# Optimization experiments

Measured on AMD Instinct MI355X. Metric: run time of the kernel, lower is better.

Reference implementation:

```python
import jax, jax.numpy as jnp
import numpy as np

B, S, D = 4, 128, 4096
H, KV, HD = 32, 8, 128
REP = H // KV  # GQA repeat factor = 4


def setup_inputs() -> dict:
    key = jax.random.key(0)
    ks = jax.random.split(key, 10)
    scale = 0.02
    x = jax.random.normal(ks[0], (B, S, D), dtype=jnp.float32)
    # projection weights stored as (in, out) so y = x @ W + b (== torch Linear)
    wq = jax.random.normal(ks[1], (D, H * HD), dtype=jnp.float32) * scale
    bq = jax.random.normal(ks[2], (H * HD,), dtype=jnp.float32) * scale
    wk = jax.random.normal(ks[3], (D, KV * HD), dtype=jnp.float32) * scale
    bk = jax.random.normal(ks[4], (KV * HD,), dtype=jnp.float32) * scale
    wv = jax.random.normal(ks[5], (D, KV * HD), dtype=jnp.float32) * scale
    bv = jax.random.normal(ks[6], (KV * HD,), dtype=jnp.float32) * scale
    wo = jax.random.normal(ks[7], (H * HD, D), dtype=jnp.float32) * scale
    bo = jax.random.normal(ks[8], (D,), dtype=jnp.float32) * scale
    # rotary frequencies: theta=10000, half-dim = HD//2 = 64
    inv_freq = 1.0 / (10000.0 ** (jnp.arange(0, HD, 2, dtype=jnp.float32) / HD))
    t = jnp.arange(S, dtype=jnp.float32)
    angles = jnp.outer(t, inv_freq)  # (S, 64)
    freqs_cos = jnp.cos(angles)
    freqs_sin = jnp.sin(angles)
    # additive causal mask (S, S): 0 on/below diagonal, -inf above
    mask = jnp.where(jnp.tril(jnp.ones((S, S), dtype=bool)), 0.0, -jnp.inf).astype(jnp.float32)
    cache_k = jnp.zeros((B, S, KV, HD), dtype=jnp.float32)
    cache_v = jnp.zeros((B, S, KV, HD), dtype=jnp.float32)
    return {
        "x": x, "start_pos": 0, "freqs_cos": freqs_cos, "freqs_sin": freqs_sin,
        "mask": mask, "cache_k": cache_k, "cache_v": cache_v,
        "wq": wq, "bq": bq, "wk": wk, "bk": bk, "wv": wv, "bv": bv,
        "wo": wo, "bo": bo,
    }


def _rope(t, cos, sin):
    # t: (B, S, h, HD); treat last dim as HD//2 complex pairs (real, imag)
    tr = t.reshape(*t.shape[:-1], HD // 2, 2)
    tre, tim = tr[..., 0], tr[..., 1]
    c = cos[None, :, None, :]  # (1, S, 1, HD//2)
    s = sin[None, :, None, :]
    out_re = tre * c - tim * s
    out_im = tre * s + tim * c
    return jnp.stack([out_re, out_im], axis=-1).reshape(t.shape)


def reference(x, start_pos, freqs_cos, freqs_sin, mask, cache_k, cache_v,
              wq, bq, wk, bk, wv, bv, wo, bo):
    bsz, seq_len, _ = x.shape
    q = (x @ wq + bq).reshape(bsz, seq_len, H, HD)
    k = (x @ wk + bk).reshape(bsz, seq_len, KV, HD)
    v = (x @ wv + bv).reshape(bsz, seq_len, KV, HD)
    q = _rope(q, freqs_cos, freqs_sin)
    k = _rope(k, freqs_cos, freqs_sin)
    # KV-cache append (functional)
    cache_k = cache_k.at[:bsz, start_pos:start_pos + seq_len].set(k)
    cache_v = cache_v.at[:bsz, start_pos:start_pos + seq_len].set(v)
    keys = cache_k[:bsz, :start_pos + seq_len]    # (B, T, KV, HD)
    vals = cache_v[:bsz, :start_pos + seq_len]
    # GQA head expansion (repeat_interleave on head dim)
    keys = jnp.repeat(keys, REP, axis=2)          # (B, T, H, HD)
    vals = jnp.repeat(vals, REP, axis=2)
    scale = 1.0 / jnp.sqrt(jnp.float32(HD))
    scores = jnp.einsum('bqhd,bkhd->bhqk', q, keys) * scale + mask
    attn = jax.nn.softmax(scores, axis=-1)
    out = jnp.einsum('bhqk,bkhd->bqhd', attn, vals).reshape(bsz, seq_len, H * HD)
    return out @ wo + bo
```

## Files before the change

kernel.cpp:

```cpp
#include <hip/hip_runtime.h>
#include <math.h>


#define B_   4
#define S_   128
#define D_   4096
#define H_   32
#define KV_  8
#define HD_  128
#define M_   (B_ * S_)
#define NQKV 6144
#define SCALE_ 0.088388347648318447f

typedef _Float16 half_t;
typedef half_t f16x8 __attribute__((ext_vector_type(8)));
typedef float  f32x4 __attribute__((ext_vector_type(4)));

__device__ inline void load_lds16(const void* g, void* l) {
    __builtin_amdgcn_global_load_lds((const __attribute__((address_space(1))) void*)g,
                                     (__attribute__((address_space(3))) void*)l,
                                     16, 0, 0);
}

__global__ void convert_f16(const float* __restrict__ in, half_t* __restrict__ out,
                            int total4) {
    int i = blockIdx.x * 256 + threadIdx.x;
    if (i >= total4) return;
    float4 f = ((const float4*)in)[i];
    __align__(8) half_t h4[4] = {(half_t)f.x, (half_t)f.y, (half_t)f.z, (half_t)f.w};
    ((uint2*)out)[i] = *(uint2*)h4;
}

__global__ __launch_bounds__(256)
void transpose_wf16(const float* __restrict__ wq, const float* __restrict__ wk,
                    const float* __restrict__ wv, half_t* __restrict__ Wt) {
    __shared__ __align__(16) float tile[64][132];
    const int t = threadIdx.x;
    const int nt = blockIdx.x, k0 = blockIdx.y * 64;
    const float* src; int Nsrc, nsrc0, ndst0;
    if (nt < 32)      { src = wq; Nsrc = 4096; nsrc0 = nt * 128;        ndst0 = nt * 128; }
    else if (nt < 40) { src = wk; Nsrc = 1024; nsrc0 = (nt - 32) * 128; ndst0 = 4096 + (nt - 32) * 128; }
    else              { src = wv; Nsrc = 1024; nsrc0 = (nt - 40) * 128; ndst0 = 5120 + (nt - 40) * 128; }
#pragma unroll
    for (int p = 0; p < 8; ++p) {
        int idx = t + p * 256;
        int r = idx >> 5, c4 = idx & 31;
        *(float4*)&tile[r][c4 * 4] =
            *(const float4*)&src[(size_t)(k0 + r) * Nsrc + nsrc0 + c4 * 4];
    }
    __syncthreads();
    const int n = t >> 1, kh = t & 1;
    __align__(16) half_t hs[32];
#pragma unroll
    for (int i = 0; i < 32; ++i)
        hs[i] = (half_t)tile[kh * 32 + i][n];
    size_t ob = (size_t)(ndst0 + n) * 4096 + k0 + kh * 32;
#pragma unroll
    for (int u = 0; u < 4; ++u)
        *(uint4*)&Wt[ob + u * 8] = *(uint4*)&hs[u * 8];
}

__global__ __launch_bounds__(256, 3)
void gemm_f16(const half_t* __restrict__ A16, const half_t* __restrict__ Bt,
              float* __restrict__ Part, int N, int K, int kslice) {
    __shared__ __align__(16) half_t As[128][64];
    __shared__ __align__(16) half_t Bs[128][64];
    const int tid = threadIdx.x;
    const int m0 = blockIdx.y * 128, n0 = blockIdx.x * 128;
    const int kbase = blockIdx.z * kslice;
    const int lane = tid & 63;
    const int quad = lane >> 4, l16 = lane & 15;
    const int w = tid >> 6;
    const int wm = (w & 1) * 64, wn = (w >> 1) * 64;
    const int tB = tid & 192;

    f32x4 acc[4][4] = {};

    for (int kc = kbase; kc < kbase + kslice; kc += 64) {
#pragma unroll
        for (int p = 0; p < 4; ++p) {
            int tb = p * 256 + tB;
            int task = tb + lane;
            int r = task >> 3;
            int os = (task ^ r) & 7;
            load_lds16(&A16[(size_t)(m0 + r) * K + kc + os * 8], (half_t*)As + tb * 8);
            load_lds16(&Bt [(size_t)(n0 + r) * K + kc + os * 8], (half_t*)Bs + tb * 8);
        }
        __syncthreads();
#pragma unroll
        for (int kk = 0; kk < 2; ++kk) {
            f16x8 af[4], bf[4];
#pragma unroll
            for (int i = 0; i < 4; ++i) {
                int ra = wm + i * 16 + l16;
                int rb = wn + i * 16 + l16;
                int L = kk * 4 + quad;
                af[i] = *(const f16x8*)&As[ra][(L ^ (ra & 7)) * 8];
                bf[i] = *(const f16x8*)&Bs[rb][(L ^ (rb & 7)) * 8];
            }
#pragma unroll
            for (int i = 0; i < 4; ++i)
#pragma unroll
                for (int j = 0; j < 4; ++j)
                    acc[i][j] = __builtin_amdgcn_mfma_f32_16x16x32_f16(af[i], bf[j], acc[i][j], 0, 0, 0);
        }
        __syncthreads();
    }
    float* Cp = Part + (size_t)blockIdx.z * ((size_t)M_ * N);
#pragma unroll
    for (int i = 0; i < 4; ++i)
#pragma unroll
        for (int j = 0; j < 4; ++j) {
            int col = n0 + wn + j * 16 + l16;
            int rowb = m0 + wm + i * 16 + quad * 4;
#pragma unroll
            for (int rg = 0; rg < 4; ++rg)
                Cp[(size_t)(rowb + rg) * N + col] = acc[i][j][rg];
        }
}

__global__ void qkv_reduce_rope(const float* __restrict__ Part, int nz,
                                const float* __restrict__ bq, const float* __restrict__ bk,
                                const float* __restrict__ bv,
                                const float* __restrict__ fc, const float* __restrict__ fs,
                                half_t* __restrict__ q16, half_t* __restrict__ k16,
                                half_t* __restrict__ vt16) {
    const int row = blockIdx.y;
    const int col = (blockIdx.x * 256 + threadIdx.x) * 2;
    const size_t off = (size_t)row * NQKV + col;
    float2 s = *(const float2*)&Part[off];
    for (int z = 1; z < nz; ++z) {
        float2 p = *(const float2*)&Part[(size_t)z * (M_ * NQKV) + off];
        s.x += p.x; s.y += p.y;
    }
    float2 bi;
    if (col < 4096)      bi = *(const float2*)&bq[col];
    else if (col < 5120) bi = *(const float2*)&bk[col - 4096];
    else                 bi = *(const float2*)&bv[col - 5120];
    s.x += bi.x; s.y += bi.y;
    if (col < 5120) {
        int d2 = (col >> 1) & 63;
        int i = row & 127;
        float c = fc[i * 64 + d2], sn = fs[i * 64 + d2];
        float re = s.x, im = s.y;
        s.x = re * c - im * sn;
        s.y = re * sn + im * c;
    }
    __align__(4) half_t hh[2] = {(half_t)s.x, (half_t)s.y};
    if (col < 4096) {
        *(unsigned int*)&q16[(size_t)row * 4096 + col] = *(unsigned int*)hh;
    } else if (col < 5120) {
        *(unsigned int*)&k16[(size_t)row * 1024 + (col - 4096)] = *(unsigned int*)hh;
    } else {
        int c = col - 5120;
        int kv = c >> 7, d = c & 127;
        int b = row >> 7, i = row & 127;
        size_t base = ((size_t)(b * 8 + kv) * 128 + d) * 128 + i;
        vt16[base]       = hh[0];
        vt16[base + 128] = hh[1];
    }
}

__global__ __launch_bounds__(256, 2)
void fused_attn(const half_t* __restrict__ q16, const half_t* __restrict__ k16,
                const half_t* __restrict__ vt16, half_t* __restrict__ a16) {
    __shared__ __align__(16) half_t Qs[32][136];
    __shared__ __align__(16) half_t Ks[128][136];
    __shared__ float Ps[32][132];
    __shared__ float red[32][16];

    const int tid = threadIdx.x;
    const int qi = blockIdx.x & 3, h = (blockIdx.x >> 2) & 31, b = blockIdx.x >> 7;
    const int kv = h >> 2;
    const int qbase = qi * 32;
    const int lane = tid & 63, w = tid >> 6;
    const int quad = lane >> 4, l16 = lane & 15;
    const int m0 = (w & 1) * 16, half64 = (w >> 1) * 64;

#pragma unroll
    for (int p = 0; p < 2; ++p) {
        int task = tid + p * 256;
        int r = task >> 4, c = task & 15;
        *(uint4*)&Qs[r][c * 8] =
            *(const uint4*)&q16[((size_t)(b * 128 + qbase + r) * 32 + h) * 128 + c * 8];
    }
#pragma unroll
    for (int p = 0; p < 8; ++p) {
        int task = tid + p * 256;
        int r = task >> 4, c = task & 15;
        *(uint4*)&Ks[r][c * 8] =
            *(const uint4*)&k16[((size_t)(b * 128 + r) * 8 + kv) * 128 + c * 8];
    }
    __syncthreads();

    f32x4 s[4] = {};
#pragma unroll
    for (int kc = 0; kc < 4; ++kc) {
        f16x8 af = *(const f16x8*)&Qs[m0 + l16][kc * 32 + quad * 8];
#pragma unroll
        for (int jb = 0; jb < 4; ++jb) {
            f16x8 bf = *(const f16x8*)&Ks[half64 + jb * 16 + l16][kc * 32 + quad * 8];
            s[jb] = __builtin_amdgcn_mfma_f32_16x16x32_f16(af, bf, s[jb], 0, 0, 0);
        }
    }
#pragma unroll
    for (int jb = 0; jb < 4; ++jb) {
        int j = half64 + jb * 16 + l16;
#pragma unroll
        for (int rg = 0; rg < 4; ++rg) {
            int row = m0 + quad * 4 + rg;
            Ps[row][j] = (j <= qbase + row) ? s[jb][rg] * SCALE_ : -1e30f;
        }
    }
    __syncthreads();

    const int r = tid >> 3, seg = tid & 7;
    float mx = -1e30f;
#pragma unroll
    for (int i = 0; i < 16; ++i) mx = fmaxf(mx, Ps[r][seg * 16 + i]);
    red[r][seg] = mx;
    __syncthreads();

    uint4 vstage[8];
#pragma unroll
    for (int p = 0; p < 8; ++p) {
        int task = tid + p * 256;
        int rr = task >> 4, c = task & 15;
        vstage[p] = *(const uint4*)&vt16[((size_t)(b * 8 + kv) * 128 + rr) * 128 + c * 8];
    }
    float m = red[r][0];
#pragma unroll
    for (int i = 1; i < 8; ++i) m = fmaxf(m, red[r][i]);
    float sum = 0.f;
#pragma unroll
    for (int i = 0; i < 16; ++i) {
        float e = __expf(Ps[r][seg * 16 + i] - m);
        Ps[r][seg * 16 + i] = e;
        sum += e;
    }
    red[r][8 + seg] = sum;
#pragma unroll
    for (int p = 0; p < 8; ++p) {
        int task = tid + p * 256;
        int rr = task >> 4, c = task & 15;
        *(uint4*)&Ks[rr][c * 8] = vstage[p];
    }
    __syncthreads();

    float tot = 0.f;
#pragma unroll
    for (int i = 0; i < 8; ++i) tot += red[r][8 + i];
    float inv = 1.0f / tot;
#pragma unroll
    for (int i = 0; i < 16; ++i)
        Qs[r][seg * 16 + i] = (half_t)(Ps[r][seg * 16 + i] * inv);
    __syncthreads();

    f32x4 o[4] = {};
#pragma unroll
    for (int jc = 0; jc < 4; ++jc) {
        f16x8 af = *(const f16x8*)&Qs[m0 + l16][jc * 32 + quad * 8];
#pragma unroll
        for (int db = 0; db < 4; ++db) {
            f16x8 bf = *(const f16x8*)&Ks[half64 + db * 16 + l16][jc * 32 + quad * 8];
            o[db] = __builtin_amdgcn_mfma_f32_16x16x32_f16(af, bf, o[db], 0, 0, 0);
        }
    }
#pragma unroll
    for (int db = 0; db < 4; ++db) {
        int d = half64 + db * 16 + l16;
#pragma unroll
        for (int rg = 0; rg < 4; ++rg) {
            int row = m0 + quad * 4 + rg;
            a16[(size_t)(b * 128 + qbase + row) * 4096 + h * 128 + d] = (half_t)o[db][rg];
        }
    }
}

__global__ void o_reduce(const float* __restrict__ Part, int nz,
                         const float* __restrict__ bo, float* __restrict__ out) {
    const size_t off = (size_t)(blockIdx.x * 256 + threadIdx.x) * 4;
    float4 s = *(const float4*)&Part[off];
    for (int z = 1; z < nz; ++z) {
        float4 p = *(const float4*)&Part[(size_t)z * (M_ * 4096) + off];
        s.x += p.x; s.y += p.y; s.z += p.z; s.w += p.w;
    }
    float4 b = *(const float4*)&bo[off & 4095];
    s.x += b.x; s.y += b.y; s.z += b.z; s.w += b.w;
    *(float4*)&out[off] = s;
}

extern "C" void kernel_launch(void* const* d_in, const int* in_sizes, int n_in,
                              void* d_out, int out_size, void* d_ws, size_t ws_size,
                              hipStream_t stream) {
    const float* x    = (const float*)d_in[0];
    const float* fc   = (const float*)d_in[2];
    const float* fs   = (const float*)d_in[3];
    const float* wq   = (const float*)d_in[7];
    const float* bq   = (const float*)d_in[8];
    const float* wk   = (const float*)d_in[9];
    const float* bk   = (const float*)d_in[10];
    const float* wv   = (const float*)d_in[11];
    const float* bv   = (const float*)d_in[12];
    const float* wo   = (const float*)d_in[13];
    const float* bo   = (const float*)d_in[14];
    float* out = (float*)d_out;

    half_t* x16  = (half_t*)d_ws;
    half_t* a16  = x16 + 2097152;
    half_t* q16  = a16 + 2097152;
    half_t* k16  = q16 + 2097152;
    half_t* vt16 = k16 + 524288;
    half_t* Wt   = vt16 + 524288;
    float*  Part = (float*)(Wt + 25165824);

    const int z = (ws_size >= (size_t)65011712 + (size_t)4 * 12582912) ? 4 : 2;
    const int kslice = 4096 / z;

    transpose_wf16<<<dim3(48, 64), 256, 0, stream>>>(wq, wk, wv, Wt);
    convert_f16<<<2048, 256, 0, stream>>>(x, x16, 524288);
    gemm_f16<<<dim3(48, 4, z), 256, 0, stream>>>(x16, Wt, Part, NQKV, 4096, kslice);
    qkv_reduce_rope<<<dim3(12, 512), 256, 0, stream>>>(Part, z, bq, bk, bv, fc, fs,
                                                       q16, k16, vt16);
    fused_attn<<<512, 256, 0, stream>>>(q16, k16, vt16, a16);

    transpose_wf16<<<dim3(32, 64), 256, 0, stream>>>(wo, wo, wo, Wt);
    gemm_f16<<<dim3(32, 4, z), 256, 0, stream>>>(a16, Wt, Part, 4096, 4096, kslice);
    o_reduce<<<2048, 256, 0, stream>>>(Part, z, bo, out);
}
```

Measured before the change: 303.9 us.

## Fuse weight transpose with x conversion and overlap Wo transpose with QKV GEMM

Merges the QKV weight transpose and the x fp16 conversion into one launch. The Wo transpose now runs as extra blocks inside the QKV GEMM launch, so it can fill idle CUs while the 192*z GEMM tiles run. Transposed weights are stored in K-slab-major layout (64-wide K slabs), which makes each GEMM B-tile load a contiguous 16 KB block. The goal is fewer launches and less idle GPU time, at the cost of a larger workspace for a separate Wo buffer, with a fallback path when the workspace is too small.

Result: faster. 293.1 us (-3.5%).

```diff
diff --git a/kernel.cpp b/kernel.cpp
--- a/kernel.cpp
+++ b/kernel.cpp
@@ -22,25 +22,11 @@
                                      16, 0, 0);
 }
 
-__global__ void convert_f16(const float* __restrict__ in, half_t* __restrict__ out,
-                            int total4) {
-    int i = blockIdx.x * 256 + threadIdx.x;
-    if (i >= total4) return;
-    float4 f = ((const float4*)in)[i];
-    __align__(8) half_t h4[4] = {(half_t)f.x, (half_t)f.y, (half_t)f.z, (half_t)f.w};
-    ((uint2*)out)[i] = *(uint2*)h4;
-}
-
-__global__ __launch_bounds__(256)
-void transpose_wf16(const float* __restrict__ wq, const float* __restrict__ wk,
-                    const float* __restrict__ wv, half_t* __restrict__ Wt) {
-    __shared__ __align__(16) float tile[64][132];
+__device__ void transpose_tile(const float* __restrict__ src, int Nsrc, int nsrc0,
+                               int ndst0, int k0, int Ntot,
+                               half_t* __restrict__ Wt, void* ldsraw) {
+    float (*tile)[132] = (float(*)[132])ldsraw;
     const int t = threadIdx.x;
-    const int nt = blockIdx.x, k0 = blockIdx.y * 64;
-    const float* src; int Nsrc, nsrc0, ndst0;
-    if (nt < 32)      { src = wq; Nsrc = 4096; nsrc0 = nt * 128;        ndst0 = nt * 128; }
-    else if (nt < 40) { src = wk; Nsrc = 1024; nsrc0 = (nt - 32) * 128; ndst0 = 4096 + (nt - 32) * 128; }
-    else              { src = wv; Nsrc = 1024; nsrc0 = (nt - 40) * 128; ndst0 = 5120 + (nt - 40) * 128; }
 #pragma unroll
     for (int p = 0; p < 8; ++p) {
         int idx = t + p * 256;
@@ -54,20 +40,19 @@
 #pragma unroll
     for (int i = 0; i < 32; ++i)
         hs[i] = (half_t)tile[kh * 32 + i][n];
-    size_t ob = (size_t)(ndst0 + n) * 4096 + k0 + kh * 32;
+    size_t ob = ((size_t)(k0 >> 6) * Ntot + ndst0 + n) * 64 + kh * 32;
 #pragma unroll
     for (int u = 0; u < 4; ++u)
         *(uint4*)&Wt[ob + u * 8] = *(uint4*)&hs[u * 8];
 }
 
-__global__ __launch_bounds__(256, 3)
-void gemm_f16(const half_t* __restrict__ A16, const half_t* __restrict__ Bt,
-              float* __restrict__ Part, int N, int K, int kslice) {
-    __shared__ __align__(16) half_t As[128][64];
-    __shared__ __align__(16) half_t Bs[128][64];
+__device__ void gemm_tile(const half_t* __restrict__ A16, const half_t* __restrict__ Wt,
+                          float* __restrict__ Part, int N, int m0, int n0,
+                          int zi, int kslice, char* lds) {
+    half_t (*As)[64] = (half_t(*)[64])lds;
+    half_t (*Bs)[64] = (half_t(*)[64])(lds + 16384);
     const int tid = threadIdx.x;
-    const int m0 = blockIdx.y * 128, n0 = blockIdx.x * 128;
-    const int kbase = blockIdx.z * kslice;
+    const int kbase = zi * kslice;
     const int lane = tid & 63;
     const int quad = lane >> 4, l16 = lane & 15;
     const int w = tid >> 6;
@@ -77,14 +62,15 @@
     f32x4 acc[4][4] = {};
 
     for (int kc = kbase; kc < kbase + kslice; kc += 64) {
+        const half_t* Bslab = Wt + ((size_t)(kc >> 6) * N + n0) * 64;
 #pragma unroll
         for (int p = 0; p < 4; ++p) {
             int tb = p * 256 + tB;
             int task = tb + lane;
             int r = task >> 3;
             int os = (task ^ r) & 7;
-            load_lds16(&A16[(size_t)(m0 + r) * K + kc + os * 8], (half_t*)As + tb * 8);
-            load_lds16(&Bt [(size_t)(n0 + r) * K + kc + os * 8], (half_t*)Bs + tb * 8);
+            load_lds16(&A16[(size_t)(m0 + r) * 4096 + kc + os * 8], (half_t*)As + tb * 8);
+            load_lds16(&Bslab[(size_t)r * 64 + os * 8],             (half_t*)Bs + tb * 8);
         }
         __syncthreads();
 #pragma unroll
@@ -106,7 +92,7 @@
         }
         __syncthreads();
     }
-    float* Cp = Part + (size_t)blockIdx.z * ((size_t)M_ * N);
+    float* Cp = Part + (size_t)zi * ((size_t)M_ * N);
 #pragma unroll
     for (int i = 0; i < 4; ++i)
 #pragma unroll
@@ -117,6 +103,62 @@
             for (int rg = 0; rg < 4; ++rg)
                 Cp[(size_t)(rowb + rg) * N + col] = acc[i][j][rg];
         }
+}
+
+__global__ __launch_bounds__(256)
+void prep_qkv(const float* __restrict__ wq, const float* __restrict__ wk,
+              const float* __restrict__ wv, const float* __restrict__ x,
+              half_t* __restrict__ Wt, half_t* __restrict__ x16) {
+    __shared__ __align__(16) char lds[33792];
+    const int bx = blockIdx.x;
+    if (bx < 3072) {
+        int nt = bx % 48, kt = bx / 48;
+        const float* src; int Nsrc, ns0, nd0;
+        if (nt < 32)      { src = wq; Nsrc = 4096; ns0 = nt * 128;        nd0 = nt * 128; }
+        else if (nt < 40) { src = wk; Nsrc = 1024; ns0 = (nt - 32) * 128; nd0 = 4096 + (nt - 32) * 128; }
+        else              { src = wv; Nsrc = 1024; ns0 = (nt - 40) * 128; nd0 = 5120 + (nt - 40) * 128; }
+        transpose_tile(src, Nsrc, ns0, nd0, kt * 64, NQKV, Wt, lds);
+    } else {
+        int i0 = (bx - 3072) * 1024 + threadIdx.x;
+#pragma unroll
+        for (int j = 0; j < 4; ++j) {
+            int i = i0 + j * 256;
+            float4 f = ((const float4*)x)[i];
+            __align__(8) half_t h4[4] = {(half_t)f.x, (half_t)f.y, (half_t)f.z, (half_t)f.w};
+            ((uint2*)x16)[i] = *(uint2*)h4;
+        }
+    }
+}
+
+__global__ __launch_bounds__(256, 3)
+void gemm_qkv_pack(const half_t* __restrict__ x16, const half_t* __restrict__ Wt,
+                   float* __restrict__ Part, int kslice, int gemmBlocks,
+                   const float* __restrict__ wo, half_t* __restrict__ WtO) {
+    __shared__ __align__(16) char lds[33792];
+    const int bx = blockIdx.x;
+    if (bx < gemmBlocks) {
+        int nb = bx % 48, mb = (bx / 48) & 3, zi = bx / 192;
+        gemm_tile(x16, Wt, Part, NQKV, mb * 128, nb * 128, zi, kslice, lds);
+    } else {
+        int t = bx - gemmBlocks;
+        int nt = t & 31, kt = t >> 5;
+        transpose_tile(wo, 4096, nt * 128, nt * 128, kt * 64, 4096, WtO, lds);
+    }
+}
+
+__global__ __launch_bounds__(256)
+void wo_trans(const float* __restrict__ wo, half_t* __restrict__ WtO) {
+    __shared__ __align__(16) char lds[33792];
+    int nt = blockIdx.x & 31, kt = blockIdx.x >> 5;
+    transpose_tile(wo, 4096, nt * 128, nt * 128, kt * 64, 4096, WtO, lds);
+}
+
+__global__ __launch_bounds__(256, 3)
+void gemm_o(const half_t* __restrict__ a16, const half_t* __restrict__ WtO,
+            float* __restrict__ Part, int kslice) {
+    __shared__ __align__(16) char lds[33792];
+    gemm_tile(a16, WtO, Part, 4096, blockIdx.y * 128, blockIdx.x * 128,
+              blockIdx.z, kslice, lds);
 }
 
 __global__ void qkv_reduce_rope(const float* __restrict__ Part, int nz,
@@ -312,19 +354,30 @@
     half_t* k16  = q16 + 2097152;
     half_t* vt16 = k16 + 524288;
     half_t* Wt   = vt16 + 524288;
-    float*  Part = (float*)(Wt + 25165824);
-
-    const int z = (ws_size >= (size_t)65011712 + (size_t)4 * 12582912) ? 4 : 2;
+
+    const size_t fixedB = 65011712;
+    const size_t fixedA = fixedB + (size_t)16777216 * 2;
+    int z; bool packed;
+    if      (ws_size >= fixedA + 4 * (size_t)12582912) { packed = true;  z = 4; }
+    else if (ws_size >= fixedA + 2 * (size_t)12582912) { packed = true;  z = 2; }
+    else if (ws_size >= fixedB + 4 * (size_t)12582912) { packed = false; z = 4; }
+    else                                               { packed = false; z = 2; }
+    half_t* WtO  = packed ? Wt + 25165824 : Wt;
+    float*  Part = (float*)((char*)d_ws + (packed ? fixedA : fixedB));
     const int kslice = 4096 / z;
 
-    transpose_wf16<<<dim3(48, 64), 256, 0, stream>>>(wq, wk, wv, Wt);
-    convert_f16<<<2048, 256, 0, stream>>>(x, x16, 524288);
-    gemm_f16<<<dim3(48, 4, z), 256, 0, stream>>>(x16, Wt, Part, NQKV, 4096, kslice);
+    prep_qkv<<<3584, 256, 0, stream>>>(wq, wk, wv, x, Wt, x16);
+
+    gemm_qkv_pack<<<192 * z + (packed ? 2048 : 0), 256, 0, stream>>>(
+        x16, Wt, Part, kslice, 192 * z, wo, WtO);
+
     qkv_reduce_rope<<<dim3(12, 512), 256, 0, stream>>>(Part, z, bq, bk, bv, fc, fs,
                                                        q16, k16, vt16);
+    if (!packed)
+        wo_trans<<<2048, 256, 0, stream>>>(wo, WtO);
+
     fused_attn<<<512, 256, 0, stream>>>(q16, k16, vt16, a16);
 
-    transpose_wf16<<<dim3(32, 64), 256, 0, stream>>>(wo, wo, wo, Wt);
-    gemm_f16<<<dim3(32, 4, z), 256, 0, stream>>>(a16, Wt, Part, 4096, 4096, kslice);
+    gemm_o<<<dim3(32, 4, z), 256, 0, stream>>>(a16, WtO, Part, kslice);
     o_reduce<<<2048, 256, 0, stream>>>(Part, z, bo, out);
 }
```
